# Optimization experiments

Hardware: AMD Instinct MI355X
Metric: run time of the kernel (lower is better)

Reference implementation:

```python
import jax, jax.numpy as jnp
import numpy as np

DIM, HEADS, K = 128, 4, 7
HD = DIM // HEADS


def _nbr_idx(n, k):
    # NATTEN boundary-clamped neighborhood (dilation=1): window start clamped to [0, n-k]
    i = np.arange(n)
    start = np.clip(i - k // 2, 0, n - k)
    idx = start[:, None] + np.arange(k)[None, :]          # (n, k) absolute neighbor index
    rel = idx - i[:, None] + (k - 1)                      # (n, k) index into 2k-1 rpb axis
    return jnp.asarray(idx), jnp.asarray(rel)


def _ln(x, w, b, eps=1e-5):
    mu = jnp.mean(x, -1, keepdims=True)
    var = jnp.var(x, -1, keepdims=True)
    return (x - mu) * jax.lax.rsqrt(var + eps) * w + b


def setup_inputs() -> dict:
    key = jax.random.key(0)
    ks = jax.random.split(key, 16)
    B, H, W, C = 1, 128, 128, DIM
    f = jax.random.normal
    inp = {
        'x': f(ks[0], (B, H, W, C), jnp.float32),
        'y': f(ks[1], (B, H, W, C), jnp.float32),
        'qv_w': f(ks[2], (2 * C, C), jnp.float32) * 0.02,
        'qv_b': jnp.zeros((2 * C,), jnp.float32),
        'k_w': f(ks[3], (C, C), jnp.float32) * 0.02,
        'k_b': jnp.zeros((C,), jnp.float32),
        'rpb': f(ks[4], (HEADS, 2 * K - 1, 2 * K - 1), jnp.float32) * 0.02,
        'proj_w': f(ks[5], (C, C), jnp.float32) * 0.02,
        'proj_b': jnp.zeros((C,), jnp.float32),
        'n1_w': jnp.ones((C,), jnp.float32),
        'n1_b': jnp.zeros((C,), jnp.float32),
        'n2_w': jnp.ones((C,), jnp.float32),
        'n2_b': jnp.zeros((C,), jnp.float32),
        'fc1_w': f(ks[6], (4 * C, C), jnp.float32) * 0.02,
        'fc1_b': jnp.zeros((4 * C,), jnp.float32),
        'fc2_w': f(ks[7], (C, 4 * C), jnp.float32) * 0.02,
        'fc2_b': jnp.zeros((C,), jnp.float32),
    }
    return inp


def _block(x, y, qv_w, qv_b, k_w, k_b, rpb, proj_w, proj_b,
           n1_w, n1_b, n2_w, n2_b, fc1_w, fc1_b, fc2_w, fc2_b):
    B, H, W, C = x.shape
    scale = HD ** -0.5
    # ---- CrossNat2D attention on norm1(x) vs y ----
    xn = _ln(x, n1_w, n1_b)
    qv = xn @ qv_w.T + qv_b                               # (B,H,W,2C)
    q = qv[..., :C].reshape(B, H, W, HEADS, HD) * scale
    v = qv[..., C:].reshape(B, H, W, HEADS, HD)
    k = (y @ k_w.T + k_b).reshape(B, H, W, HEADS, HD)

    idx_h, rel_h = _nbr_idx(H, K)
    idx_w, rel_w = _nbr_idx(W, K)
    # gather neighborhoods: (B, H, K, W, K, HEADS, HD)
    k_nbr = k[:, idx_h][:, :, :, idx_w]
    v_nbr = v[:, idx_h][:, :, :, idx_w]

    # attention logits over KxK neighborhood
    attn = jnp.einsum('bijhd,biajchd->bijhac', q, k_nbr)  # (B,H,W,heads,K,K)
    bias = rpb[:, rel_h][..., rel_w]                      # (heads,H,K,W,K)
    attn = attn + jnp.transpose(bias, (1, 3, 0, 2, 4))    # broadcast over B
    attn = jax.nn.softmax(attn.reshape(B, H, W, HEADS, K * K), axis=-1)
    attn = attn.reshape(B, H, W, HEADS, K, K)

    out = jnp.einsum('bijhac,biajchd->bijhd', attn, v_nbr).reshape(B, H, W, C)
    out = out @ proj_w.T + proj_b

    x = x + out
    # ---- MLP ----
    h = _ln(x, n2_w, n2_b) @ fc1_w.T + fc1_b
    h = jax.nn.gelu(h, approximate=False) @ fc2_w.T + fc2_b
    return x + h


def reference(x, y, qv_w, qv_b, k_w, k_b, rpb, proj_w, proj_b,
              n1_w, n1_b, n2_w, n2_b, fc1_w, fc1_b, fc2_w, fc2_b):
    return _block(x, y, qv_w, qv_b, k_w, k_b, rpb, proj_w, proj_b,
                  n1_w, n1_b, n2_w, n2_b, fc1_w, fc1_b, fc2_w, fc2_b)
```

## Files before the change

kernel.cpp:

```cpp
#include <hip/hip_runtime.h>
#include <hip/hip_bf16.h>


#define N_PIX 16384
#define C 128
#define HEADS 4
#define HD 32
#define HW 128

typedef __hip_bfloat16 bf16;
typedef __attribute__((ext_vector_type(8))) short bf16x8;
typedef __attribute__((ext_vector_type(4))) float f32x4;

__device__ __forceinline__ float b2f(bf16 v) { return __bfloat162float(v); }
__device__ __forceinline__ short f2bs(float f) {
    bf16 h = __float2bfloat16(f);
    return (short)__bfloat16_as_ushort(h);
}
__device__ __forceinline__ float bs2f(short s) {
    __hip_bfloat16_raw r; r.x = (unsigned short)s;
    return __bfloat162float(__hip_bfloat16(r));
}

__global__ __launch_bounds__(256) void k_wconv(
    const float* __restrict__ qv_w, const float* __restrict__ k_w,
    const float* __restrict__ proj_w, const float* __restrict__ fc1_w,
    const float* __restrict__ fc2_w,
    short* __restrict__ wqv, short* __restrict__ wk, short* __restrict__ wproj,
    short* __restrict__ wfc1, short* __restrict__ wfc2) {
    const int i = blockIdx.x * 256 + threadIdx.x;
    if (i < 32768) wqv[i] = f2bs(qv_w[i]);
    if (i < 16384) { wk[i] = f2bs(k_w[i]); wproj[i] = f2bs(proj_w[i]); }
    if (i < 65536) { wfc1[i] = f2bs(fc1_w[i]); wfc2[i] = f2bs(fc2_w[i]); }
}

__global__ __launch_bounds__(512, 6) void k_qkv(
    const float* __restrict__ x, const float* __restrict__ y,
    const short* __restrict__ wqv, const float* __restrict__ qv_b,
    const short* __restrict__ wk, const float* __restrict__ k_b,
    const float* __restrict__ n1_w, const float* __restrict__ n1_b,
    bf16* __restrict__ qb, bf16* __restrict__ vb, bf16* __restrict__ kb) {
    __shared__ float xr[32][132];
    __shared__ short xn[32][136];
    __shared__ short yb[32][136];
    __shared__ float redS[32][8], redQ[32][8];
    __shared__ float muA[32], riA[32];
    const int t = threadIdx.x;
    const int pix0 = blockIdx.x * 32;
    for (int e = t; e < 32 * 128; e += 512) {
        const int r = e >> 7, c = e & 127;
        xr[r][c] = x[(pix0 + r) * C + c];
        yb[r][c] = f2bs(y[(pix0 + r) * C + c]);
    }
    __syncthreads();
    if (t < 256) {
        const int r = t >> 3, s = t & 7;
        float sm = 0.f, sq = 0.f;
        for (int i = 0; i < 16; i++) { float v = xr[r][s * 16 + i]; sm += v; sq += v * v; }
        redS[r][s] = sm; redQ[r][s] = sq;
    }
    __syncthreads();
    if (t < 32) {
        float sm = 0.f, sq = 0.f;
        for (int s = 0; s < 8; s++) { sm += redS[t][s]; sq += redQ[t][s]; }
        const float mu = sm * (1.f / 128.f);
        const float var = sq * (1.f / 128.f) - mu * mu;
        muA[t] = mu; riA[t] = rsqrtf(var + 1e-5f);
    }
    __syncthreads();
    for (int e = t; e < 32 * 128; e += 512) {
        const int r = e >> 7, c = e & 127;
        xn[r][c] = f2bs((xr[r][c] - muA[r]) * riA[r] * n1_w[c] + n1_b[c]);
    }
    __syncthreads();
    const int wave = t >> 6, lane = t & 63, quad = lane >> 4, l15 = lane & 15;
    const float scale = 0.1767766952966369f;
    for (int jt = wave; jt < 48; jt += 8) {
        const int mt = jt & 1, nt = jt >> 1;
        f32x4 acc = {0.f, 0.f, 0.f, 0.f};
        if (nt < 16) {
            const int n = nt * 16 + l15;
            for (int kt = 0; kt < 4; kt++) {
                bf16x8 a = *(const bf16x8*)&xn[mt * 16 + l15][kt * 32 + quad * 8];
                bf16x8 b = *(const bf16x8*)&wqv[n * C + kt * 32 + quad * 8];
                acc = __builtin_amdgcn_mfma_f32_16x16x32_bf16(a, b, acc, 0, 0, 0);
            }
            const float bias = qv_b[n];
            for (int r = 0; r < 4; r++) {
                const int m = mt * 16 + quad * 4 + r;
                const float v = acc[r] + bias;
                if (n < C) qb[(pix0 + m) * C + n] = __float2bfloat16(v * scale);
                else       vb[(pix0 + m) * C + (n - C)] = __float2bfloat16(v);
            }
        } else {
            const int n = (nt - 16) * 16 + l15;
            for (int kt = 0; kt < 4; kt++) {
                bf16x8 a = *(const bf16x8*)&yb[mt * 16 + l15][kt * 32 + quad * 8];
                bf16x8 b = *(const bf16x8*)&wk[n * C + kt * 32 + quad * 8];
                acc = __builtin_amdgcn_mfma_f32_16x16x32_bf16(a, b, acc, 0, 0, 0);
            }
            const float bias = k_b[n];
            for (int r = 0; r < 4; r++) {
                const int m = mt * 16 + quad * 4 + r;
                kb[(pix0 + m) * C + n] = __float2bfloat16(acc[r] + bias);
            }
        }
    }
}

__global__ __launch_bounds__(256) void k_attn(
    const bf16* qb, const bf16* __restrict__ kb,
    const bf16* __restrict__ vb, const float* __restrict__ rpb,
    bf16* ao) {
    __shared__ short KP[100 * 132];
    __shared__ short Vl[100 * 132];
    const int t = threadIdx.x;
    const int h = t >> 6, lane = t & 63, quad = lane >> 4, l15 = lane & 15;
    const int i0 = (blockIdx.x >> 5) * 4;
    const int j0 = (blockIdx.x & 31) * 4;
    const int rs = min(max(i0 - 3, 0), 118);
    const int cs = min(max(j0 - 3, 0), 118);
    for (int u = t; u < 100 * 16 * 2; u += 256) {
        const int tv = (u >= 1600) ? 1 : 0;
        const int uu = tv ? u - 1600 : u;
        const int r = uu >> 4, seg = uu & 15;
        const int wr = r / 10, wc = r % 10;
        const size_t g = (size_t)((rs + wr) * HW + cs + wc) * C + seg * 8;
        const uint4 d = *(const uint4*)((tv ? vb : kb) + g);
        *(uint4*)&(tv ? Vl : KP)[r * 132 + seg * 8] = d;
    }
    __syncthreads();
    const int pA = (i0 + (l15 >> 2)) * HW + j0 + (l15 & 3);
    const bf16x8 aQ = *(const bf16x8*)(qb + (size_t)pA * C + h * HD + quad * 8);
    f32x4 S[7];
    int aiL[7], ajL[7]; bool inb[7];
    for (int nt = 0; nt < 7; nt++) {
        const int nb = nt * 16 + l15;
        aiL[nt] = rs + nb / 10;
        ajL[nt] = cs + nb % 10;
        inb[nt] = nb < 100;
        const bf16x8 bK = *(const bf16x8*)&KP[(nt * 16 + l15) * 132 + h * HD + quad * 8];
        f32x4 z = {0.f, 0.f, 0.f, 0.f};
        S[nt] = __builtin_amdgcn_mfma_f32_16x16x32_bf16(aQ, bK, z, 0, 0, 0);
    }
    const float* rpbh = rpb + h * 169;
    float sm[4];
    for (int r = 0; r < 4; r++) {
        const int m = quad * 4 + r;
        const int i = i0 + (m >> 2), j = j0 + (m & 3);
        const int shi = min(max(i - 3, 0), 121);
        const int swj = min(max(j - 3, 0), 121);
        float best = -1e30f;
        for (int nt = 0; nt < 7; nt++) {
            const int ai = aiL[nt], aj = ajL[nt];
            const bool valid = inb[nt] & (ai >= shi) & (ai <= shi + 6) & (aj >= swj) & (aj <= swj + 6);
            const int ri = min(max(ai - i + 6, 0), 12);
            const int rj = min(max(aj - j + 6, 0), 12);
            const float v = valid ? (S[nt][r] + rpbh[ri * 13 + rj]) : -1e30f;
            S[nt][r] = v;
            best = fmaxf(best, v);
        }
        for (int msk = 1; msk < 16; msk <<= 1) best = fmaxf(best, __shfl_xor(best, msk, 64));
        float s = 0.f;
        for (int nt = 0; nt < 7; nt++) {
            const float e = __expf(S[nt][r] - best);
            S[nt][r] = e;
            s += e;
        }
        for (int msk = 1; msk < 16; msk <<= 1) s += __shfl_xor(s, msk, 64);
        sm[r] = 1.f / s;
    }
    __syncthreads();
    for (int r = 0; r < 4; r++) {
        short* prow = &KP[(h * 16 + quad * 4 + r) * 136];
        for (int nt = 0; nt < 7; nt++)
            prow[nt * 16 + l15] = f2bs(S[nt][r] * sm[r]);
        prow[112 + l15] = 0;
    }
    __syncthreads();
    f32x4 O0 = {0.f, 0.f, 0.f, 0.f}, O1 = {0.f, 0.f, 0.f, 0.f};
    for (int kt = 0; kt < 4; kt++) {
        const bf16x8 aP = *(const bf16x8*)&KP[(h * 16 + l15) * 136 + kt * 32 + quad * 8];
        for (int nt2 = 0; nt2 < 2; nt2++) {
            bf16x8 bV;
            const int ch = h * HD + nt2 * 16 + l15;
#pragma unroll
            for (int jj = 0; jj < 8; jj++) {
                const int nbr = kt * 32 + quad * 8 + jj;
                bV[jj] = (nbr < 100) ? Vl[nbr * 132 + ch] : (short)0;
            }
            if (nt2 == 0) O0 = __builtin_amdgcn_mfma_f32_16x16x32_bf16(aP, bV, O0, 0, 0, 0);
            else          O1 = __builtin_amdgcn_mfma_f32_16x16x32_bf16(aP, bV, O1, 0, 0, 0);
        }
    }
    for (int r = 0; r < 4; r++) {
        const int m = quad * 4 + r;
        const int p = (i0 + (m >> 2)) * HW + j0 + (m & 3);
        ao[(size_t)p * C + h * HD + l15] = __float2bfloat16(O0[r]);
        ao[(size_t)p * C + h * HD + 16 + l15] = __float2bfloat16(O1[r]);
    }
}

__global__ __launch_bounds__(512, 6) void k_mlp2(
    const float* __restrict__ x, const bf16* __restrict__ ao,
    const short* __restrict__ wproj, const float* __restrict__ proj_b,
    const float* __restrict__ n2_w, const float* __restrict__ n2_b,
    const short* __restrict__ wfc1, const float* __restrict__ fc1_b,
    const short* __restrict__ wfc2, const float* __restrict__ fc2_b,
    float* __restrict__ out) {
    __shared__ short x1b[32][136];
    __shared__ short xn[32][136];
    __shared__ short hb[32][520];
    __shared__ float redS[32][8], redQ[32][8];
    __shared__ float muA[32], riA[32];
    const int t = threadIdx.x;
    const int pix0 = blockIdx.x * 32;
    const int wave = t >> 6, lane = t & 63, quad = lane >> 4, l15 = lane & 15;
    for (int jt = wave; jt < 16; jt += 8) {
        const int mt = jt >> 3, nt = jt & 7;
        const int n = nt * 16 + l15;
        const bf16* aop = ao + (size_t)(pix0 + mt * 16 + l15) * C;
        f32x4 acc = {0.f, 0.f, 0.f, 0.f};
        for (int kt = 0; kt < 4; kt++) {
            bf16x8 a = *(const bf16x8*)(aop + kt * 32 + quad * 8);
            bf16x8 b = *(const bf16x8*)&wproj[n * C + kt * 32 + quad * 8];
            acc = __builtin_amdgcn_mfma_f32_16x16x32_bf16(a, b, acc, 0, 0, 0);
        }
        const float bias = proj_b[n];
        for (int r = 0; r < 4; r++) {
            const int m = mt * 16 + quad * 4 + r;
            x1b[m][n] = f2bs(x[(pix0 + m) * C + n] + acc[r] + bias);
        }
    }
    __syncthreads();
    if (t < 256) {
        const int r = t >> 3, s = t & 7;
        float sm = 0.f, sq = 0.f;
        for (int i = 0; i < 16; i++) { float v = bs2f(x1b[r][s * 16 + i]); sm += v; sq += v * v; }
        redS[r][s] = sm; redQ[r][s] = sq;
    }
    __syncthreads();
    if (t < 32) {
        float sm = 0.f, sq = 0.f;
        for (int s = 0; s < 8; s++) { sm += redS[t][s]; sq += redQ[t][s]; }
        const float mu = sm * (1.f / 128.f);
        const float var = sq * (1.f / 128.f) - mu * mu;
        muA[t] = mu; riA[t] = rsqrtf(var + 1e-5f);
    }
    __syncthreads();
    for (int e = t; e < 32 * 128; e += 512) {
        const int r = e >> 7, c = e & 127;
        xn[r][c] = f2bs((bs2f(x1b[r][c]) - muA[r]) * riA[r] * n2_w[c] + n2_b[c]);
    }
    __syncthreads();
    for (int jt = wave; jt < 64; jt += 8) {
        const int mt = jt >> 5, nt = jt & 31;
        const int n = nt * 16 + l15;
        f32x4 acc = {0.f, 0.f, 0.f, 0.f};
        for (int kt = 0; kt < 4; kt++) {
            bf16x8 a = *(const bf16x8*)&xn[mt * 16 + l15][kt * 32 + quad * 8];
            bf16x8 b = *(const bf16x8*)&wfc1[n * C + kt * 32 + quad * 8];
            acc = __builtin_amdgcn_mfma_f32_16x16x32_bf16(a, b, acc, 0, 0, 0);
        }
        const float bias = fc1_b[n];
        for (int r = 0; r < 4; r++) {
            const int m = mt * 16 + quad * 4 + r;
            float v = acc[r] + bias;
            v = 0.5f * v * (1.f + erff(v * 0.70710678118654752f));
            hb[m][n] = f2bs(v);
        }
    }
    __syncthreads();
    for (int jt = wave; jt < 16; jt += 8) {
        const int mt = jt >> 3, nt = jt & 7;
        const int n = nt * 16 + l15;
        f32x4 acc = {0.f, 0.f, 0.f, 0.f};
        for (int kt = 0; kt < 16; kt++) {
            bf16x8 a = *(const bf16x8*)&hb[mt * 16 + l15][kt * 32 + quad * 8];
            bf16x8 b = *(const bf16x8*)&wfc2[n * 512 + kt * 32 + quad * 8];
            acc = __builtin_amdgcn_mfma_f32_16x16x32_bf16(a, b, acc, 0, 0, 0);
        }
        const float bias = fc2_b[n];
        for (int r = 0; r < 4; r++) {
            const int m = mt * 16 + quad * 4 + r;
            out[(pix0 + m) * C + n] = acc[r] + bias + bs2f(x1b[m][n]);
        }
    }
}

extern "C" void kernel_launch(void* const* d_in, const int* in_sizes, int n_in,
                              void* d_out, int out_size, void* d_ws, size_t ws_size,
                              hipStream_t stream) {
    const float* x      = (const float*)d_in[0];
    const float* y      = (const float*)d_in[1];
    const float* qv_w   = (const float*)d_in[2];
    const float* qv_b   = (const float*)d_in[3];
    const float* k_w    = (const float*)d_in[4];
    const float* k_b    = (const float*)d_in[5];
    const float* rpb    = (const float*)d_in[6];
    const float* proj_w = (const float*)d_in[7];
    const float* proj_b = (const float*)d_in[8];
    const float* n1_w   = (const float*)d_in[9];
    const float* n1_b   = (const float*)d_in[10];
    const float* n2_w   = (const float*)d_in[11];
    const float* n2_b   = (const float*)d_in[12];
    const float* fc1_w  = (const float*)d_in[13];
    const float* fc1_b  = (const float*)d_in[14];
    const float* fc2_w  = (const float*)d_in[15];
    const float* fc2_b  = (const float*)d_in[16];
    float* out = (float*)d_out;

    bf16* qb  = (bf16*)d_ws;
    bf16* vb  = qb + (size_t)N_PIX * C;
    bf16* kb  = vb + (size_t)N_PIX * C;
    short* wqv  = (short*)(kb + (size_t)N_PIX * C);
    short* wk   = wqv + 32768;
    short* wproj= wk + 16384;
    short* wfc1 = wproj + 16384;
    short* wfc2 = wfc1 + 65536;
    bf16* ao = qb;

    k_wconv<<<256, 256, 0, stream>>>(qv_w, k_w, proj_w, fc1_w, fc2_w,
                                     wqv, wk, wproj, wfc1, wfc2);
    k_qkv<<<N_PIX / 32, 512, 0, stream>>>(x, y, wqv, qv_b, wk, k_b, n1_w, n1_b, qb, vb, kb);
    k_attn<<<1024, 256, 0, stream>>>(qb, kb, vb, rpb, ao);
    k_mlp2<<<N_PIX / 32, 512, 0, stream>>>(x, ao, wproj, proj_b, n2_w, n2_b,
                                           wfc1, fc1_b, wfc2, fc2_b, out);
}
```

Before: 176.2 us.

## Fuse LayerNorm and QKV projection into neighborhood attention kernel with halo recompute

Merges the QKV projection kernel into the attention kernel. Each 4x4 tile block loads its 10x10 halo of x and y, computes LayerNorm, the K and V projections for all halo pixels and Q for its own pixels directly into shared memory. This removes the global q/k/v intermediate buffers and one launch. The cost is redundant recomputation of K/V and LayerNorm for overlapping halos, plus higher LDS and register use per block.

```diff
diff --git a/kernel.cpp b/kernel.cpp
--- a/kernel.cpp
+++ b/kernel.cpp
@@ -20,6 +20,10 @@
 __device__ __forceinline__ float bs2f(short s) {
     __hip_bfloat16_raw r; r.x = (unsigned short)s;
     return __bfloat162float(__hip_bfloat16(r));
+}
+__device__ __forceinline__ float wave_sum(float v) {
+    for (int m = 1; m < 64; m <<= 1) v += __shfl_xor(v, m, 64);
+    return v;
 }
 
 __global__ __launch_bounds__(256) void k_wconv(
@@ -34,104 +38,122 @@
     if (i < 65536) { wfc1[i] = f2bs(fc1_w[i]); wfc2[i] = f2bs(fc2_w[i]); }
 }
 
-__global__ __launch_bounds__(512, 6) void k_qkv(
+__global__ __launch_bounds__(256) void k_fused(
     const float* __restrict__ x, const float* __restrict__ y,
     const short* __restrict__ wqv, const float* __restrict__ qv_b,
     const short* __restrict__ wk, const float* __restrict__ k_b,
     const float* __restrict__ n1_w, const float* __restrict__ n1_b,
-    bf16* __restrict__ qb, bf16* __restrict__ vb, bf16* __restrict__ kb) {
-    __shared__ float xr[32][132];
-    __shared__ short xn[32][136];
-    __shared__ short yb[32][136];
-    __shared__ float redS[32][8], redQ[32][8];
-    __shared__ float muA[32], riA[32];
+    const float* __restrict__ rpb, bf16* __restrict__ ao) {
+    __shared__ short U[112 * 136];
+    __shared__ short KP[112 * 136];
+    __shared__ short Qb[16 * 136];
+    __shared__ float redS[100][2], redQ[100][2];
+    __shared__ float muA[100], riA[100];
     const int t = threadIdx.x;
-    const int pix0 = blockIdx.x * 32;
-    for (int e = t; e < 32 * 128; e += 512) {
-        const int r = e >> 7, c = e & 127;
-        xr[r][c] = x[(pix0 + r) * C + c];
-        yb[r][c] = f2bs(y[(pix0 + r) * C + c]);
-    }
-    __syncthreads();
-    if (t < 256) {
-        const int r = t >> 3, s = t & 7;
-        float sm = 0.f, sq = 0.f;
-        for (int i = 0; i < 16; i++) { float v = xr[r][s * 16 + i]; sm += v; sq += v * v; }
-        redS[r][s] = sm; redQ[r][s] = sq;
-    }
-    __syncthreads();
-    if (t < 32) {
-        float sm = 0.f, sq = 0.f;
-        for (int s = 0; s < 8; s++) { sm += redS[t][s]; sq += redQ[t][s]; }
-        const float mu = sm * (1.f / 128.f);
-        const float var = sq * (1.f / 128.f) - mu * mu;
-        muA[t] = mu; riA[t] = rsqrtf(var + 1e-5f);
-    }
-    __syncthreads();
-    for (int e = t; e < 32 * 128; e += 512) {
-        const int r = e >> 7, c = e & 127;
-        xn[r][c] = f2bs((xr[r][c] - muA[r]) * riA[r] * n1_w[c] + n1_b[c]);
-    }
-    __syncthreads();
     const int wave = t >> 6, lane = t & 63, quad = lane >> 4, l15 = lane & 15;
-    const float scale = 0.1767766952966369f;
-    for (int jt = wave; jt < 48; jt += 8) {
-        const int mt = jt & 1, nt = jt >> 1;
-        f32x4 acc = {0.f, 0.f, 0.f, 0.f};
-        if (nt < 16) {
-            const int n = nt * 16 + l15;
-            for (int kt = 0; kt < 4; kt++) {
-                bf16x8 a = *(const bf16x8*)&xn[mt * 16 + l15][kt * 32 + quad * 8];
-                bf16x8 b = *(const bf16x8*)&wqv[n * C + kt * 32 + quad * 8];
-                acc = __builtin_amdgcn_mfma_f32_16x16x32_bf16(a, b, acc, 0, 0, 0);
-            }
-            const float bias = qv_b[n];
-            for (int r = 0; r < 4; r++) {
-                const int m = mt * 16 + quad * 4 + r;
-                const float v = acc[r] + bias;
-                if (n < C) qb[(pix0 + m) * C + n] = __float2bfloat16(v * scale);
-                else       vb[(pix0 + m) * C + (n - C)] = __float2bfloat16(v);
-            }
-        } else {
-            const int n = (nt - 16) * 16 + l15;
-            for (int kt = 0; kt < 4; kt++) {
-                bf16x8 a = *(const bf16x8*)&yb[mt * 16 + l15][kt * 32 + quad * 8];
-                bf16x8 b = *(const bf16x8*)&wk[n * C + kt * 32 + quad * 8];
-                acc = __builtin_amdgcn_mfma_f32_16x16x32_bf16(a, b, acc, 0, 0, 0);
-            }
-            const float bias = k_b[n];
-            for (int r = 0; r < 4; r++) {
-                const int m = mt * 16 + quad * 4 + r;
-                kb[(pix0 + m) * C + n] = __float2bfloat16(acc[r] + bias);
-            }
-        }
-    }
-}
-
-__global__ __launch_bounds__(256) void k_attn(
-    const bf16* qb, const bf16* __restrict__ kb,
-    const bf16* __restrict__ vb, const float* __restrict__ rpb,
-    bf16* ao) {
-    __shared__ short KP[100 * 132];
-    __shared__ short Vl[100 * 132];
-    const int t = threadIdx.x;
-    const int h = t >> 6, lane = t & 63, quad = lane >> 4, l15 = lane & 15;
+    const int h = wave;
     const int i0 = (blockIdx.x >> 5) * 4;
     const int j0 = (blockIdx.x & 31) * 4;
     const int rs = min(max(i0 - 3, 0), 118);
     const int cs = min(max(j0 - 3, 0), 118);
-    for (int u = t; u < 100 * 16 * 2; u += 256) {
-        const int tv = (u >= 1600) ? 1 : 0;
-        const int uu = tv ? u - 1600 : u;
-        const int r = uu >> 4, seg = uu & 15;
-        const int wr = r / 10, wc = r % 10;
-        const size_t g = (size_t)((rs + wr) * HW + cs + wc) * C + seg * 8;
-        const uint4 d = *(const uint4*)((tv ? vb : kb) + g);
-        *(uint4*)&(tv ? Vl : KP)[r * 132 + seg * 8] = d;
-    }
-    __syncthreads();
-    const int pA = (i0 + (l15 >> 2)) * HW + j0 + (l15 & 3);
-    const bf16x8 aQ = *(const bf16x8*)(qb + (size_t)pA * C + h * HD + quad * 8);
+    for (int u = t; u < 112 * 16; u += 256) {
+        const int r = u >> 4, seg = u & 15;
+        if (r < 100) {
+            const int gi = rs + r / 10, gj = cs + r % 10;
+            const float* yp = y + (size_t)(gi * HW + gj) * C + seg * 8;
+            bf16x8 tmp;
+#pragma unroll
+            for (int jj = 0; jj < 8; jj++) tmp[jj] = f2bs(yp[jj]);
+            *(bf16x8*)&U[r * 136 + seg * 8] = tmp;
+        } else {
+            bf16x8 z = {0, 0, 0, 0, 0, 0, 0, 0};
+            *(bf16x8*)&U[r * 136 + seg * 8] = z;
+            *(bf16x8*)&KP[r * 136 + seg * 8] = z;
+        }
+    }
+    for (int base = 0; base < 100; base += 2) {
+        const int r = base + (wave >> 1);
+        const int cc = (wave & 1) * 64 + lane;
+        const int gi = rs + r / 10, gj = cs + r % 10;
+        const float v = x[(size_t)(gi * HW + gj) * C + cc];
+        const float s = wave_sum(v);
+        const float q = wave_sum(v * v);
+        if (lane == 0) { redS[r][wave & 1] = s; redQ[r][wave & 1] = q; }
+    }
+    __syncthreads();
+    if (t < 100) {
+        const float sm = redS[t][0] + redS[t][1];
+        const float sq = redQ[t][0] + redQ[t][1];
+        const float mu = sm * (1.f / 128.f);
+        const float var = sq * (1.f / 128.f) - mu * mu;
+        muA[t] = mu; riA[t] = rsqrtf(var + 1e-5f);
+    }
+    for (int jt = wave; jt < 56; jt += 4) {
+        const int mt = jt >> 3, nt = jt & 7;
+        const int n = nt * 16 + l15;
+        f32x4 acc = {0.f, 0.f, 0.f, 0.f};
+        for (int kt = 0; kt < 4; kt++) {
+            bf16x8 a = *(const bf16x8*)&U[(mt * 16 + l15) * 136 + kt * 32 + quad * 8];
+            bf16x8 b = *(const bf16x8*)&wk[n * C + kt * 32 + quad * 8];
+            acc = __builtin_amdgcn_mfma_f32_16x16x32_bf16(a, b, acc, 0, 0, 0);
+        }
+        const float bias = k_b[n];
+        for (int r = 0; r < 4; r++) {
+            const int row = mt * 16 + quad * 4 + r;
+            if (row < 100) KP[row * 136 + n] = f2bs(acc[r] + bias);
+        }
+    }
+    __syncthreads();
+    for (int e = t; e < 100 * 128; e += 256) {
+        const int r = e >> 7, c = e & 127;
+        const int gi = rs + r / 10, gj = cs + r % 10;
+        const float v = x[(size_t)(gi * HW + gj) * C + c];
+        U[r * 136 + c] = f2bs((v - muA[r]) * riA[r] * n1_w[c] + n1_b[c]);
+    }
+    __syncthreads();
+    const float scale = 0.1767766952966369f;
+    const int urow_own = (i0 + (l15 >> 2) - rs) * 10 + (j0 + (l15 & 3) - cs);
+#pragma unroll
+    for (int qi = 0; qi < 2; qi++) {
+        const int nt = wave * 2 + qi, n = nt * 16 + l15;
+        f32x4 acc = {0.f, 0.f, 0.f, 0.f};
+        for (int kt = 0; kt < 4; kt++) {
+            bf16x8 a = *(const bf16x8*)&U[urow_own * 136 + kt * 32 + quad * 8];
+            bf16x8 b = *(const bf16x8*)&wqv[n * C + kt * 32 + quad * 8];
+            acc = __builtin_amdgcn_mfma_f32_16x16x32_bf16(a, b, acc, 0, 0, 0);
+        }
+        const float bias = qv_b[n];
+        for (int r = 0; r < 4; r++)
+            Qb[(quad * 4 + r) * 136 + n] = f2bs((acc[r] + bias) * scale);
+    }
+    f32x4 Vacc[14];
+#pragma unroll
+    for (int j2 = 0; j2 < 14; j2++) {
+        const int jt = j2 * 4 + wave;
+        const int mt = jt >> 3, nt = jt & 7;
+        const int n = nt * 16 + l15;
+        f32x4 acc = {0.f, 0.f, 0.f, 0.f};
+        for (int kt = 0; kt < 4; kt++) {
+            bf16x8 a = *(const bf16x8*)&U[(mt * 16 + l15) * 136 + kt * 32 + quad * 8];
+            bf16x8 b = *(const bf16x8*)&wqv[(size_t)(128 + n) * C + kt * 32 + quad * 8];
+            acc = __builtin_amdgcn_mfma_f32_16x16x32_bf16(a, b, acc, 0, 0, 0);
+        }
+        Vacc[j2] = acc;
+    }
+    __syncthreads();
+#pragma unroll
+    for (int j2 = 0; j2 < 14; j2++) {
+        const int jt = j2 * 4 + wave;
+        const int mt = jt >> 3, nt = jt & 7;
+        const int n = nt * 16 + l15;
+        const float bias = qv_b[128 + n];
+        for (int r = 0; r < 4; r++) {
+            const int row = mt * 16 + quad * 4 + r;
+            if (row < 100) U[row * 136 + n] = f2bs(Vacc[j2][r] + bias);
+        }
+    }
+    __syncthreads();
+    const bf16x8 aQ = *(const bf16x8*)&Qb[l15 * 136 + h * HD + quad * 8];
     f32x4 S[7];
     int aiL[7], ajL[7]; bool inb[7];
     for (int nt = 0; nt < 7; nt++) {
@@ -139,7 +161,7 @@
         aiL[nt] = rs + nb / 10;
         ajL[nt] = cs + nb % 10;
         inb[nt] = nb < 100;
-        const bf16x8 bK = *(const bf16x8*)&KP[(nt * 16 + l15) * 132 + h * HD + quad * 8];
+        const bf16x8 bK = *(const bf16x8*)&KP[(nt * 16 + l15) * 136 + h * HD + quad * 8];
         f32x4 z = {0.f, 0.f, 0.f, 0.f};
         S[nt] = __builtin_amdgcn_mfma_f32_16x16x32_bf16(aQ, bK, z, 0, 0, 0);
     }
@@ -187,7 +209,7 @@
 #pragma unroll
             for (int jj = 0; jj < 8; jj++) {
                 const int nbr = kt * 32 + quad * 8 + jj;
-                bV[jj] = (nbr < 100) ? Vl[nbr * 132 + ch] : (short)0;
+                bV[jj] = (nbr < 100) ? U[nbr * 136 + ch] : (short)0;
             }
             if (nt2 == 0) O0 = __builtin_amdgcn_mfma_f32_16x16x32_bf16(aP, bV, O0, 0, 0, 0);
             else          O1 = __builtin_amdgcn_mfma_f32_16x16x32_bf16(aP, bV, O1, 0, 0, 0);
@@ -310,20 +332,16 @@
     const float* fc2_b  = (const float*)d_in[16];
     float* out = (float*)d_out;
 
-    bf16* qb  = (bf16*)d_ws;
-    bf16* vb  = qb + (size_t)N_PIX * C;
-    bf16* kb  = vb + (size_t)N_PIX * C;
-    short* wqv  = (short*)(kb + (size_t)N_PIX * C);
+    bf16* ao = (bf16*)d_ws;
+    short* wqv  = (short*)(ao + (size_t)N_PIX * C);
     short* wk   = wqv + 32768;
     short* wproj= wk + 16384;
     short* wfc1 = wproj + 16384;
     short* wfc2 = wfc1 + 65536;
-    bf16* ao = qb;
 
     k_wconv<<<256, 256, 0, stream>>>(qv_w, k_w, proj_w, fc1_w, fc2_w,
                                      wqv, wk, wproj, wfc1, wfc2);
-    k_qkv<<<N_PIX / 32, 512, 0, stream>>>(x, y, wqv, qv_b, wk, k_b, n1_w, n1_b, qb, vb, kb);
-    k_attn<<<1024, 256, 0, stream>>>(qb, kb, vb, rpb, ao);
+    k_fused<<<1024, 256, 0, stream>>>(x, y, wqv, qv_b, wk, k_b, n1_w, n1_b, rpb, ao);
     k_mlp2<<<N_PIX / 32, 512, 0, stream>>>(x, ao, wproj, proj_b, n2_w, n2_b,
                                            wfc1, fc1_b, wfc2, fc2_b, out);
 }
```

Measured after the change: 250.1 us. 42.0% more time.

## Split neighborhood attention into one single-wave block per head and tile

Applied to the files above, without the earlier changes.

The attention kernel moves from one 256-thread block covering all four heads of a 4x4 pixel tile to one 64-thread block per (tile, head), launching 4096 blocks. Each block now stages only its head's 32 channels of K and V, so shared memory per block drops from roughly 52 KB to roughly 20 KB, and probability rows get their own small buffer. Because each block is a single wavefront, the __syncthreads barriers are removed. Several loops, including the fc2 K-loop in the MLP kernel, also get explicit unroll pragmas. The intent is higher occupancy and less barrier stalling, at the cost of relying on in-wave LDS ordering without a barrier and issuing more, smaller global loads.

```diff
diff --git a/kernel.cpp b/kernel.cpp
--- a/kernel.cpp
+++ b/kernel.cpp
@@ -108,49 +108,52 @@
     }
 }
 
-__global__ __launch_bounds__(256) void k_attn(
+__global__ __launch_bounds__(64) void k_attn(
     const bf16* qb, const bf16* __restrict__ kb,
     const bf16* __restrict__ vb, const float* __restrict__ rpb,
     bf16* ao) {
-    __shared__ short KP[100 * 132];
-    __shared__ short Vl[100 * 132];
+    __shared__ short Kl[112 * 36];
+    __shared__ short Vl[112 * 36];
+    __shared__ short Pl[16 * 136];
     const int t = threadIdx.x;
-    const int h = t >> 6, lane = t & 63, quad = lane >> 4, l15 = lane & 15;
-    const int i0 = (blockIdx.x >> 5) * 4;
-    const int j0 = (blockIdx.x & 31) * 4;
+    const int quad = t >> 4, l15 = t & 15;
+    const int tile = blockIdx.x >> 2, h = blockIdx.x & 3;
+    const int i0 = (tile >> 5) * 4;
+    const int j0 = (tile & 31) * 4;
     const int rs = min(max(i0 - 3, 0), 118);
     const int cs = min(max(j0 - 3, 0), 118);
-    for (int u = t; u < 100 * 16 * 2; u += 256) {
-        const int tv = (u >= 1600) ? 1 : 0;
-        const int uu = tv ? u - 1600 : u;
-        const int r = uu >> 4, seg = uu & 15;
-        const int wr = r / 10, wc = r % 10;
-        const size_t g = (size_t)((rs + wr) * HW + cs + wc) * C + seg * 8;
+    for (int u = t; u < 800; u += 64) {
+        const int tv = (u >= 400) ? 1 : 0;
+        const int uu = tv ? u - 400 : u;
+        const int r = uu >> 2, seg = uu & 3;
+        const size_t g = (size_t)((rs + r / 10) * HW + cs + r % 10) * C + h * HD + seg * 8;
         const uint4 d = *(const uint4*)((tv ? vb : kb) + g);
-        *(uint4*)&(tv ? Vl : KP)[r * 132 + seg * 8] = d;
-    }
-    __syncthreads();
+        *(uint4*)&(tv ? Vl : Kl)[r * 36 + seg * 8] = d;
+    }
     const int pA = (i0 + (l15 >> 2)) * HW + j0 + (l15 & 3);
     const bf16x8 aQ = *(const bf16x8*)(qb + (size_t)pA * C + h * HD + quad * 8);
     f32x4 S[7];
     int aiL[7], ajL[7]; bool inb[7];
+#pragma unroll
     for (int nt = 0; nt < 7; nt++) {
         const int nb = nt * 16 + l15;
         aiL[nt] = rs + nb / 10;
         ajL[nt] = cs + nb % 10;
         inb[nt] = nb < 100;
-        const bf16x8 bK = *(const bf16x8*)&KP[(nt * 16 + l15) * 132 + h * HD + quad * 8];
+        const bf16x8 bK = *(const bf16x8*)&Kl[(nt * 16 + l15) * 36 + quad * 8];
         f32x4 z = {0.f, 0.f, 0.f, 0.f};
         S[nt] = __builtin_amdgcn_mfma_f32_16x16x32_bf16(aQ, bK, z, 0, 0, 0);
     }
     const float* rpbh = rpb + h * 169;
     float sm[4];
+#pragma unroll
     for (int r = 0; r < 4; r++) {
         const int m = quad * 4 + r;
         const int i = i0 + (m >> 2), j = j0 + (m & 3);
         const int shi = min(max(i - 3, 0), 121);
         const int swj = min(max(j - 3, 0), 121);
         float best = -1e30f;
+#pragma unroll
         for (int nt = 0; nt < 7; nt++) {
             const int ai = aiL[nt], aj = ajL[nt];
             const bool valid = inb[nt] & (ai >= shi) & (ai <= shi + 6) & (aj >= swj) & (aj <= swj + 6);
@@ -162,6 +165,7 @@
         }
         for (int msk = 1; msk < 16; msk <<= 1) best = fmaxf(best, __shfl_xor(best, msk, 64));
         float s = 0.f;
+#pragma unroll
         for (int nt = 0; nt < 7; nt++) {
             const float e = __expf(S[nt][r] - best);
             S[nt][r] = e;
@@ -170,29 +174,32 @@
         for (int msk = 1; msk < 16; msk <<= 1) s += __shfl_xor(s, msk, 64);
         sm[r] = 1.f / s;
     }
-    __syncthreads();
+#pragma unroll
     for (int r = 0; r < 4; r++) {
-        short* prow = &KP[(h * 16 + quad * 4 + r) * 136];
+        short* prow = &Pl[(quad * 4 + r) * 136];
+#pragma unroll
         for (int nt = 0; nt < 7; nt++)
             prow[nt * 16 + l15] = f2bs(S[nt][r] * sm[r]);
         prow[112 + l15] = 0;
     }
-    __syncthreads();
     f32x4 O0 = {0.f, 0.f, 0.f, 0.f}, O1 = {0.f, 0.f, 0.f, 0.f};
+#pragma unroll
     for (int kt = 0; kt < 4; kt++) {
-        const bf16x8 aP = *(const bf16x8*)&KP[(h * 16 + l15) * 136 + kt * 32 + quad * 8];
+        const bf16x8 aP = *(const bf16x8*)&Pl[l15 * 136 + kt * 32 + quad * 8];
+#pragma unroll
         for (int nt2 = 0; nt2 < 2; nt2++) {
             bf16x8 bV;
-            const int ch = h * HD + nt2 * 16 + l15;
+            const int ch = nt2 * 16 + l15;
 #pragma unroll
             for (int jj = 0; jj < 8; jj++) {
                 const int nbr = kt * 32 + quad * 8 + jj;
-                bV[jj] = (nbr < 100) ? Vl[nbr * 132 + ch] : (short)0;
+                bV[jj] = (nbr < 100) ? Vl[nbr * 36 + ch] : (short)0;
             }
             if (nt2 == 0) O0 = __builtin_amdgcn_mfma_f32_16x16x32_bf16(aP, bV, O0, 0, 0, 0);
             else          O1 = __builtin_amdgcn_mfma_f32_16x16x32_bf16(aP, bV, O1, 0, 0, 0);
         }
     }
+#pragma unroll
     for (int r = 0; r < 4; r++) {
         const int m = quad * 4 + r;
         const int p = (i0 + (m >> 2)) * HW + j0 + (m & 3);
@@ -275,6 +282,7 @@
         const int mt = jt >> 3, nt = jt & 7;
         const int n = nt * 16 + l15;
         f32x4 acc = {0.f, 0.f, 0.f, 0.f};
+#pragma unroll
         for (int kt = 0; kt < 16; kt++) {
             bf16x8 a = *(const bf16x8*)&hb[mt * 16 + l15][kt * 32 + quad * 8];
             bf16x8 b = *(const bf16x8*)&wfc2[n * 512 + kt * 32 + quad * 8];
@@ -323,7 +331,7 @@
     k_wconv<<<256, 256, 0, stream>>>(qv_w, k_w, proj_w, fc1_w, fc2_w,
                                      wqv, wk, wproj, wfc1, wfc2);
     k_qkv<<<N_PIX / 32, 512, 0, stream>>>(x, y, wqv, qv_b, wk, k_b, n1_w, n1_b, qb, vb, kb);
-    k_attn<<<1024, 256, 0, stream>>>(qb, kb, vb, rpb, ao);
+    k_attn<<<4096, 64, 0, stream>>>(qb, kb, vb, rpb, ao);
     k_mlp2<<<N_PIX / 32, 512, 0, stream>>>(x, ao, wproj, proj_b, n2_w, n2_b,
                                            wfc1, fc1_b, wfc2, fc2_b, out);
 }
```

Result: no change. 178.5 us (+1.3%).
